# Kernel optimization log

Hardware: AMD Instinct MI355X
Metric: run time of the kernel (lower is better)

## Reference

```python
import jax, jax.numpy as jnp
import numpy as np

B, N, C = 32, 256, 4096
H = 16
HEAD_DIM = C // H  # 256 == N, required by the module's math
SCALE = HEAD_DIM ** -0.5


def setup_inputs() -> dict:
    key = jax.random.key(0)
    ks = jax.random.split(key, 7)
    std = C ** -0.5
    return {
        "x1": jax.random.normal(ks[0], (B, N, C), dtype=jnp.float32),
        "x2": jax.random.normal(ks[1], (B, N, C), dtype=jnp.float32),
        "Wq": jax.random.normal(ks[2], (C, C), dtype=jnp.float32) * std,
        "Wk": jax.random.normal(ks[3], (C, C), dtype=jnp.float32) * std,
        "Wv": jax.random.normal(ks[4], (C, C), dtype=jnp.float32) * std,
        "Wp": jax.random.normal(ks[5], (C, C), dtype=jnp.float32) * std,
        "bp": jnp.zeros((C,), dtype=jnp.float32),
    }


def reference(x1, x2, Wq, Wk, Wv, Wp, bp):
    b, n, c = x1.shape
    h, hd = H, HEAD_DIM
    # QKV projections (qkv_bias=False); q pre-scaled as in source
    q = (x1 @ Wq.T) * SCALE
    k = x2 @ Wk.T
    v = x2 @ Wv.T
    split = lambda t: t.reshape(b, n, h, hd).transpose(0, 2, 1, 3)  # b h n hd
    q, k, v = split(q), split(k), split(v)
    # channel-wise attention: q^T @ k over the token axis -> [b, h, hd, hd]
    attn = jax.nn.softmax(jnp.einsum("bhni,bhnj->bhij", q, k), axis=-1)
    # attn @ v: inner dim of attn (hd) contracts with token axis of v (n == hd)
    out = jnp.einsum("bhin,bhnc->bhic", attn, v)  # [b, h, hd, hd]
    out = out.transpose(0, 2, 1, 3).reshape(b, n, c)
    x = out @ Wp.T + bp
    return (x, attn)
```

## Files before the change

kernel.cpp:

```cpp
#include <hip/hip_runtime.h>

typedef __attribute__((ext_vector_type(4))) float f32x4;
typedef __attribute__((ext_vector_type(8))) short short8;
typedef __attribute__((ext_vector_type(4))) unsigned short ushort4v;

__device__ __forceinline__ unsigned short rne_bf16(float f) {
  unsigned int u = __builtin_bit_cast(unsigned int, f);
  u += 0x7FFFu + ((u >> 16) & 1u);
  return (unsigned short)(u >> 16);
}

__device__ __forceinline__ void async16(void* lds, const void* g) {
  __builtin_amdgcn_global_load_lds(
      (const __attribute__((address_space(1))) void*)g,
      (__attribute__((address_space(3))) void*)lds, 16, 0, 0);
}

__device__ __forceinline__ f32x4 mfma16(short8 a, short8 b, f32x4 c) {
  return __builtin_amdgcn_mfma_f32_16x16x32_bf16(a, b, c, 0, 0, 0);
}

__global__ __launch_bounds__(256) void cast_k(const float* __restrict__ in,
                                              unsigned short* __restrict__ out,
                                              int n4) {
  int stride = gridDim.x * 256;
  for (int i = blockIdx.x * 256 + threadIdx.x; i < n4; i += stride) {
    float4 v = ((const float4*)in)[i];
    ushort4v o = {rne_bf16(v.x), rne_bf16(v.y), rne_bf16(v.z), rne_bf16(v.w)};
    ((ushort4v*)out)[i] = o;
  }
}

__global__ __launch_bounds__(256) void cast_all(const float* __restrict__ x1,
                                                const float* __restrict__ x2,
                                                const float* __restrict__ Wq,
                                                const float* __restrict__ Wk,
                                                const float* __restrict__ Wv,
                                                const float* __restrict__ Wp,
                                                unsigned short* __restrict__ x1b,
                                                unsigned short* __restrict__ x2b,
                                                unsigned short* __restrict__ Wb4) {
  const int stride = gridDim.x * 256;
  for (int i = blockIdx.x * 256 + threadIdx.x; i < 33554432; i += stride) {
    const float* src;
    unsigned short* dst;
    int off;
    if (i < 8388608) {
      src = x1; dst = x1b; off = i;
    } else if (i < 16777216) {
      src = x2; dst = x2b; off = i - 8388608;
    } else {
      const int w = (i - 16777216) >> 22;
      off = (i - 16777216) & 4194303;
      src = (w == 0) ? Wq : (w == 1) ? Wk : (w == 2) ? Wv : Wp;
      dst = Wb4 + (size_t)w * 16777216;
    }
    float4 v = ((const float4*)src)[off];
    ushort4v o = {rne_bf16(v.x), rne_bf16(v.y), rne_bf16(v.z), rne_bf16(v.w)};
    ((ushort4v*)dst)[off] = o;
  }
}

template <int MODE>
__global__ __launch_bounds__(512, 2) void gemm256(const unsigned short* __restrict__ A1,
                                                  const unsigned short* __restrict__ A2,
                                                  const unsigned short* __restrict__ Bb,
                                                  size_t wstride,
                                                  float* __restrict__ outF,
                                                  unsigned short* __restrict__ outB0,
                                                  const float* __restrict__ bias,
                                                  int K, int lda, int ldb,
                                                  float scale0, float scale1, int gx) {
  __shared__ unsigned short lds[65536];
  const int tid = threadIdx.x;
  const int lane = tid & 63;
  const int wid = tid >> 6;
  const int wm = wid >> 2;
  const int wn = wid & 3;
  const int z = blockIdx.z;
  const unsigned short* A = z ? A2 : A1;
  const unsigned short* B = Bb + (size_t)z * wstride;
  unsigned short* outB = (MODE == 0) ? outB0 + (size_t)z * 33554432 : outB0;
  const float scale = z ? scale1 : scale0;
  int lin = blockIdx.x;
  lin = (lin & 7) * (gridDim.x >> 3) + (lin >> 3);
  const int bx = lin % gx;
  const int by = lin / gx;
  const int m0 = by * 256, n0 = bx * 256;
  const int NT = K >> 6;

  const int gsw8 = (((tid & 3) ^ ((tid >> 3) & 3))) * 8;
  const unsigned short* gA = A + (size_t)(m0 + (tid >> 2)) * lda + gsw8;
  const unsigned short* gB = B + (size_t)(n0 + (tid >> 2)) * ldb + gsw8;
  const size_t astep = (size_t)128 * lda;
  const size_t bstep = (size_t)128 * ldb;
  unsigned short* ld0 = &lds[tid * 8];

#define STG(Q) do { \
    const int kt_ = ((Q) >> 1) * 64 + ((Q) & 1) * 32; \
    const int off_ = (((Q) >> 1) & 1) * 32768 + ((Q) & 1) * 8192; \
    const unsigned short* sA_ = gA + kt_; \
    unsigned short* dA_ = ld0 + off_; \
    async16(dA_, sA_); async16(dA_ + 4096, sA_ + astep); \
    const unsigned short* sB_ = gB + kt_; \
    unsigned short* dB_ = ld0 + 16384 + off_; \
    async16(dB_, sB_); async16(dB_ + 4096, sB_ + bstep); } while (0)

  const int rl = lane & 15;
  const int ch = (lane >> 4) ^ ((rl >> 1) & 3);
  const int aidx = wm * 4096 + rl * 32 + ch * 8;
  const int bidx = 16384 + wn * 2048 + rl * 32 + ch * 8;

  short8 af[8], bf0[4], bf1[4];
#define READ_A(base) do { \
    _Pragma("unroll") \
    for (int r_ = 0; r_ < 8; ++r_) af[r_] = *(const short8*)&lds[(base) + aidx + r_ * 512]; \
  } while (0)
#define READ_B(base, dst) do { \
    _Pragma("unroll") \
    for (int s_ = 0; s_ < 4; ++s_) dst[s_] = *(const short8*)&lds[(base) + bidx + s_ * 512]; \
  } while (0)

  f32x4 acc[8][4];
#pragma unroll
  for (int r = 0; r < 8; ++r)
#pragma unroll
    for (int s = 0; s < 4; ++s) acc[r][s] = (f32x4){0.f, 0.f, 0.f, 0.f};

#define MFMA32(bfX) do { \
    __builtin_amdgcn_s_setprio(1); \
    _Pragma("unroll") \
    for (int r_ = 0; r_ < 8; ++r_) \
      _Pragma("unroll") \
      for (int s_ = 0; s_ < 4; ++s_) acc[r_][s_] = mfma16(af[r_], bfX[s_], acc[r_][s_]); \
    __builtin_amdgcn_s_setprio(0); \
  } while (0)

  STG(0); STG(1); STG(2);
  asm volatile("s_waitcnt vmcnt(4)" ::: "memory");
  __builtin_amdgcn_s_barrier();
  READ_B(0, bf0);

  for (int t = 0; t < NT; ++t) {
    const int bb = (t & 1) * 32768;
    READ_A(bb);
    READ_B(bb + 8192, bf1);
    if (t + 1 < NT) STG(2 * t + 3);
    __builtin_amdgcn_sched_barrier(0);
    MFMA32(bf0);
    if (t + 1 < NT) asm volatile("s_waitcnt vmcnt(4)" ::: "memory");
    else            asm volatile("s_waitcnt vmcnt(0)" ::: "memory");
    __builtin_amdgcn_s_barrier();
    READ_A(bb + 8192);
    if (t + 1 < NT) {
      READ_B(((t + 1) & 1) * 32768, bf0);
      if (t + 2 < NT) STG(2 * t + 4);
    }
    __builtin_amdgcn_sched_barrier(0);
    MFMA32(bf1);
    if (t + 1 < NT) {
      if (t + 2 < NT) asm volatile("s_waitcnt vmcnt(4)" ::: "memory");
      else            asm volatile("s_waitcnt vmcnt(0)" ::: "memory");
      __builtin_amdgcn_s_barrier();
    }
  }
#undef STG
#undef READ_A
#undef READ_B
#undef MFMA32

  const int fcol = lane & 15;
  const int frow = (lane >> 4) * 4;
#pragma unroll
  for (int r = 0; r < 8; ++r) {
#pragma unroll
    for (int s = 0; s < 4; ++s) {
      f32x4 v = acc[r][s];
      const int m = m0 + wm * 128 + r * 16 + frow;
      const int n = n0 + wn * 64 + s * 16 + fcol;
      if (MODE == 0) {
        ushort4v p;
#pragma unroll
        for (int j = 0; j < 4; ++j) p[j] = rne_bf16(v[j] * scale);
        size_t d = ((size_t)((m >> 8) * 16 + (n >> 8))) * 65536 +
                   (size_t)(n & 255) * 256 + (m & 255);
        *(ushort4v*)&outB[d] = p;
      } else {
        float bv = bias[n];
#pragma unroll
        for (int j = 0; j < 4; ++j) outF[(size_t)(m + j) * 4096 + n] = v[j] + bv;
      }
    }
  }
}

__global__ __launch_bounds__(256) void attn_fused(const unsigned short* __restrict__ Qt,
                                                  const unsigned short* __restrict__ Kt,
                                                  const unsigned short* __restrict__ Vt,
                                                  float* __restrict__ outA,
                                                  unsigned short* __restrict__ outXb) {
  __shared__ unsigned short sh[34560];
  const int tid = threadIdx.x;
  const int lane = tid & 63;
  const int wid = tid >> 6;
  const int z = blockIdx.y;
  const int m0 = blockIdx.x * 64;
  const int wm = wid >> 1;
  const int wn = wid & 1;
  const int fcol = lane & 15;
  const int kslot = (lane >> 4) * 8;
  const int frow = (lane >> 4) * 4;

  const unsigned short* Qh = Qt + (size_t)z * 65536;
  const unsigned short* Kh = Kt + (size_t)z * 65536;
  const unsigned short* Vh = Vt + (size_t)z * 65536;
  float* redM = (float*)&sh[33536];
  float* redS = redM + 128;

  f32x4 acc[2][8];
#pragma unroll
  for (int r = 0; r < 2; ++r)
#pragma unroll
    for (int s = 0; s < 8; ++s) acc[r][s] = (f32x4){0.f, 0.f, 0.f, 0.f};

  {
    const int arow = tid >> 2;
    const int acol = (tid & 3) * 8;
    const unsigned short* gQ = Qh + (size_t)(m0 + arow) * 256 + acol;
    const unsigned short* gK = Kh + (size_t)arow * 256 + acol;
    unsigned short* lA = &sh[tid * 8];
    unsigned short* lB = &sh[2048 + tid * 8];

    for (int kt = 0; kt < 256; kt += 32) {
      __syncthreads();
      async16(lA, gQ + kt);
      async16(lB, gK + kt);
      async16(lB + 2048, gK + (size_t)64 * 256 + kt);
      async16(lB + 4096, gK + (size_t)128 * 256 + kt);
      async16(lB + 6144, gK + (size_t)192 * 256 + kt);
      __syncthreads();

      short8 a[2], b[8];
#pragma unroll
      for (int r = 0; r < 2; ++r)
        a[r] = *(const short8*)&sh[(wm * 32 + r * 16 + fcol) * 32 + kslot];
#pragma unroll
      for (int s = 0; s < 8; ++s)
        b[s] = *(const short8*)&sh[2048 + (wn * 128 + s * 16 + fcol) * 32 + kslot];
#pragma unroll
      for (int r = 0; r < 2; ++r)
#pragma unroll
        for (int s = 0; s < 8; ++s)
          acc[r][s] = mfma16(a[r], b[s], acc[r][s]);
    }
  }
  __syncthreads();

#pragma unroll
  for (int r = 0; r < 2; ++r) {
#pragma unroll
    for (int j = 0; j < 4; ++j) {
      float m = acc[r][0][j];
#pragma unroll
      for (int s = 1; s < 8; ++s) m = fmaxf(m, acc[r][s][j]);
#pragma unroll
      for (int off = 1; off < 16; off <<= 1) m = fmaxf(m, __shfl_xor(m, off, 64));
      if (fcol == 0) redM[(wm * 32 + r * 16 + frow + j) * 2 + wn] = m;
    }
  }
  __syncthreads();
#pragma unroll
  for (int r = 0; r < 2; ++r) {
#pragma unroll
    for (int j = 0; j < 4; ++j) {
      const int rl = wm * 32 + r * 16 + frow + j;
      const float m = fmaxf(redM[rl * 2 + 0], redM[rl * 2 + 1]);
      float sum = 0.f;
#pragma unroll
      for (int s = 0; s < 8; ++s) {
        float e = __expf(acc[r][s][j] - m);
        acc[r][s][j] = e;
        sum += e;
      }
#pragma unroll
      for (int off = 1; off < 16; off <<= 1) sum += __shfl_xor(sum, off, 64);
      if (fcol == 0) redS[rl * 2 + wn] = sum;
    }
  }
  __syncthreads();
#pragma unroll
  for (int r = 0; r < 2; ++r) {
#pragma unroll
    for (int j = 0; j < 4; ++j) {
      const int rl = wm * 32 + r * 16 + frow + j;
      const float inv = 1.0f / (redS[rl * 2 + 0] + redS[rl * 2 + 1]);
      const size_t rowo = (size_t)z * 65536 + (size_t)(m0 + rl) * 256;
#pragma unroll
      for (int s = 0; s < 8; ++s) {
        const int col = wn * 128 + s * 16 + fcol;
        const float p = acc[r][s][j] * inv;
        outA[rowo + col] = p;
        sh[16384 + rl * 268 + col] = rne_bf16(p);
      }
    }
  }
  __syncthreads();

  const unsigned short* gV = Vh + (size_t)(tid >> 2) * 256 + (tid & 3) * 8;
#define STGV(kt, vb) do { \
    _Pragma("unroll") \
    for (int k_ = 0; k_ < 4; ++k_) \
      async16(&sh[(vb) + tid * 8 + k_ * 2048], \
              gV + (size_t)k_ * 64 * 256 + (kt) * 32); } while (0)

  STGV(0, 0); STGV(1, 8192);
  asm volatile("s_waitcnt vmcnt(4)" ::: "memory");
  __builtin_amdgcn_s_barrier();

  f32x4 acc2[2][8];
#pragma unroll
  for (int r = 0; r < 2; ++r)
#pragma unroll
    for (int s = 0; s < 8; ++s) acc2[r][s] = (f32x4){0.f, 0.f, 0.f, 0.f};

  for (int kt = 0; kt < 8; ++kt) {
    const int vb = (kt & 1) * 8192;
    short8 a2[2], b2[8];
#pragma unroll
    for (int r = 0; r < 2; ++r)
      a2[r] = *(const short8*)&sh[16384 + (wm * 32 + r * 16 + fcol) * 268 + kt * 32 + kslot];
#pragma unroll
    for (int s = 0; s < 8; ++s)
      b2[s] = *(const short8*)&sh[vb + (wn * 128 + s * 16 + fcol) * 32 + kslot];
#pragma unroll
    for (int r = 0; r < 2; ++r)
#pragma unroll
      for (int s = 0; s < 8; ++s)
        acc2[r][s] = mfma16(a2[r], b2[s], acc2[r][s]);
    __builtin_amdgcn_s_barrier();
    if (kt + 2 < 8) {
      STGV(kt + 2, vb);
      asm volatile("s_waitcnt vmcnt(4)" ::: "memory");
    } else {
      asm volatile("s_waitcnt vmcnt(0)" ::: "memory");
    }
    __builtin_amdgcn_s_barrier();
  }
#undef STGV

#pragma unroll
  for (int r = 0; r < 2; ++r) {
#pragma unroll
    for (int s = 0; s < 8; ++s) {
      f32x4 v = acc2[r][s];
      const int i0 = m0 + wm * 32 + r * 16 + frow;
      const int c = wn * 128 + s * 16 + fcol;
#pragma unroll
      for (int j = 0; j < 4; ++j) {
        size_t d = ((size_t)((z >> 4) * 256 + i0 + j)) * 4096 + (z & 15) * 256 + c;
        outXb[d] = rne_bf16(v[j]);
      }
    }
  }
}

extern "C" void kernel_launch(void* const* d_in, const int* in_sizes, int n_in,
                              void* d_out, int out_size, void* d_ws, size_t ws_size,
                              hipStream_t stream) {
  const float* x1 = (const float*)d_in[0];
  const float* x2 = (const float*)d_in[1];
  const float* Wq = (const float*)d_in[2];
  const float* Wk = (const float*)d_in[3];
  const float* Wv = (const float*)d_in[4];
  const float* Wp = (const float*)d_in[5];
  const float* bp = (const float*)d_in[6];

  float* outX = (float*)d_out;
  float* outA = outX + (size_t)33554432;

  unsigned short* Qt  = (unsigned short*)d_ws;
  unsigned short* Kt  = Qt + 33554432;
  unsigned short* Vt  = Kt + 33554432;
  unsigned short* x1b = Vt + 33554432;
  unsigned short* x2b = x1b + 33554432;

  const float SCALE = 0.0625f;
  const bool big = ws_size >= 469762048ULL;

  if (big) {
    unsigned short* Wb4 = x2b + 33554432;
    cast_all<<<2048, 256, 0, stream>>>(x1, x2, Wq, Wk, Wv, Wp, x1b, x2b, Wb4);
    gemm256<0><<<dim3(512, 1, 3), 512, 0, stream>>>(
        x1b, x2b, Wb4, (size_t)16777216, nullptr, Qt, nullptr,
        4096, 4096, 4096, SCALE, 1.0f, 16);
    attn_fused<<<dim3(4, 512), 256, 0, stream>>>(Qt, Kt, Vt, outA, x2b);
    gemm256<3><<<dim3(512, 1, 1), 512, 0, stream>>>(
        x2b, x2b, Wb4 + (size_t)50331648, 0, outX, nullptr, bp,
        4096, 4096, 4096, 1.0f, 1.0f, 16);
  } else {
    unsigned short* Wb = x2b + 33554432;
    cast_k<<<2048, 256, 0, stream>>>(x1, x1b, 8388608);
    cast_k<<<2048, 256, 0, stream>>>(x2, x2b, 8388608);
    cast_k<<<2048, 256, 0, stream>>>(Wq, Wb, 4194304);
    gemm256<0><<<dim3(512, 1, 1), 512, 0, stream>>>(
        x1b, x1b, Wb, 0, nullptr, Qt, nullptr, 4096, 4096, 4096, SCALE, SCALE, 16);
    cast_k<<<2048, 256, 0, stream>>>(Wk, Wb, 4194304);
    gemm256<0><<<dim3(512, 1, 1), 512, 0, stream>>>(
        x2b, x2b, Wb, 0, nullptr, Kt, nullptr, 4096, 4096, 4096, 1.0f, 1.0f, 16);
    cast_k<<<2048, 256, 0, stream>>>(Wv, Wb, 4194304);
    gemm256<0><<<dim3(512, 1, 1), 512, 0, stream>>>(
        x2b, x2b, Wb, 0, nullptr, Vt, nullptr, 4096, 4096, 4096, 1.0f, 1.0f, 16);
    attn_fused<<<dim3(4, 512), 256, 0, stream>>>(Qt, Kt, Vt, outA, x2b);
    cast_k<<<2048, 256, 0, stream>>>(Wp, Wb, 4194304);
    gemm256<3><<<dim3(512, 1, 1), 512, 0, stream>>>(
        x2b, x2b, Wb, 0, outX, nullptr, bp, 4096, 4096, 4096, 1.0f, 1.0f, 16);
  }
}
```

Measured before the change: 1.265 ms.

## Restructure GEMM main loop into quadrant-phased MFMA with split A/B staging

Reworks the bf16 GEMM inner loop so each 64-wide K step runs as four quadrant phases (4x2 MFMA tiles over both K halves). Each phase reads a smaller set of fragments from LDS and separates them with barriers. Global-to-LDS staging is split into separate A and B loads and issued between phases, and the prologue now prefetches four stages (vmcnt 8). The aim is to lower register pressure and interleave LDS reads with MFMA work. In exchange it adds more barriers per iteration and extra LDS-wait stalls.

```diff
diff --git a/kernel.cpp b/kernel.cpp
--- a/kernel.cpp
+++ b/kernel.cpp
@@ -96,14 +96,15 @@
   const size_t bstep = (size_t)128 * ldb;
   unsigned short* ld0 = &lds[tid * 8];
 
-#define STG(Q) do { \
-    const int kt_ = ((Q) >> 1) * 64 + ((Q) & 1) * 32; \
-    const int off_ = (((Q) >> 1) & 1) * 32768 + ((Q) & 1) * 8192; \
-    const unsigned short* sA_ = gA + kt_; \
-    unsigned short* dA_ = ld0 + off_; \
-    async16(dA_, sA_); async16(dA_ + 4096, sA_ + astep); \
-    const unsigned short* sB_ = gB + kt_; \
-    unsigned short* dB_ = ld0 + 16384 + off_; \
+#define ROFF(Q) ((((Q) >> 1) & 1) * 32768 + ((Q) & 1) * 8192)
+#define RKT(Q) (((Q) >> 1) * 64 + ((Q) & 1) * 32)
+#define STG_A(Q) do { \
+    const unsigned short* sA_ = gA + RKT(Q); \
+    unsigned short* dA_ = ld0 + ROFF(Q); \
+    async16(dA_, sA_); async16(dA_ + 4096, sA_ + astep); } while (0)
+#define STG_B(Q) do { \
+    const unsigned short* sB_ = gB + RKT(Q); \
+    unsigned short* dB_ = ld0 + 16384 + ROFF(Q); \
     async16(dB_, sB_); async16(dB_ + 4096, sB_ + bstep); } while (0)
 
   const int rl = lane & 15;
@@ -111,14 +112,16 @@
   const int aidx = wm * 4096 + rl * 32 + ch * 8;
   const int bidx = 16384 + wn * 2048 + rl * 32 + ch * 8;
 
-  short8 af[8], bf0[4], bf1[4];
-#define READ_A(base) do { \
+  short8 af0[4], af1[4], b00[2], b01[2], b10[2], b11[2];
+#define READ_A4(dst, base, q) do { \
     _Pragma("unroll") \
-    for (int r_ = 0; r_ < 8; ++r_) af[r_] = *(const short8*)&lds[(base) + aidx + r_ * 512]; \
+    for (int r_ = 0; r_ < 4; ++r_) \
+      dst[r_] = *(const short8*)&lds[(base) + aidx + ((q) * 4 + r_) * 512]; \
   } while (0)
-#define READ_B(base, dst) do { \
+#define READ_B2(dst, base, h) do { \
     _Pragma("unroll") \
-    for (int s_ = 0; s_ < 4; ++s_) dst[s_] = *(const short8*)&lds[(base) + bidx + s_ * 512]; \
+    for (int s_ = 0; s_ < 2; ++s_) \
+      dst[s_] = *(const short8*)&lds[(base) + bidx + ((h) * 2 + s_) * 512]; \
   } while (0)
 
   f32x4 acc[8][4];
@@ -127,47 +130,69 @@
 #pragma unroll
     for (int s = 0; s < 4; ++s) acc[r][s] = (f32x4){0.f, 0.f, 0.f, 0.f};
 
-#define MFMA32(bfX) do { \
+#define MFMAQ(bk0, bk1, ro, so) do { \
     __builtin_amdgcn_s_setprio(1); \
     _Pragma("unroll") \
-    for (int r_ = 0; r_ < 8; ++r_) \
+    for (int r_ = 0; r_ < 4; ++r_) \
       _Pragma("unroll") \
-      for (int s_ = 0; s_ < 4; ++s_) acc[r_][s_] = mfma16(af[r_], bfX[s_], acc[r_][s_]); \
+      for (int s_ = 0; s_ < 2; ++s_) { \
+        acc[(ro) + r_][(so) + s_] = mfma16(af0[r_], bk0[s_], acc[(ro) + r_][(so) + s_]); \
+        acc[(ro) + r_][(so) + s_] = mfma16(af1[r_], bk1[s_], acc[(ro) + r_][(so) + s_]); \
+      } \
     __builtin_amdgcn_s_setprio(0); \
   } while (0)
 
-  STG(0); STG(1); STG(2);
-  asm volatile("s_waitcnt vmcnt(4)" ::: "memory");
+#define PUBLISH() do { \
+    __builtin_amdgcn_s_barrier(); \
+    asm volatile("s_waitcnt lgkmcnt(0)" ::: "memory"); \
+    __builtin_amdgcn_sched_barrier(0); \
+  } while (0)
+
+  STG_A(0); STG_B(0); STG_A(1); STG_B(1);
+  STG_A(2); STG_B(2); STG_A(3); STG_B(3);
+  asm volatile("s_waitcnt vmcnt(8)" ::: "memory");
   __builtin_amdgcn_s_barrier();
-  READ_B(0, bf0);
 
   for (int t = 0; t < NT; ++t) {
-    const int bb = (t & 1) * 32768;
-    READ_A(bb);
-    READ_B(bb + 8192, bf1);
-    if (t + 1 < NT) STG(2 * t + 3);
-    __builtin_amdgcn_sched_barrier(0);
-    MFMA32(bf0);
-    if (t + 1 < NT) asm volatile("s_waitcnt vmcnt(4)" ::: "memory");
-    else            asm volatile("s_waitcnt vmcnt(0)" ::: "memory");
-    __builtin_amdgcn_s_barrier();
-    READ_A(bb + 8192);
-    if (t + 1 < NT) {
-      READ_B(((t + 1) & 1) * 32768, bf0);
-      if (t + 2 < NT) STG(2 * t + 4);
-    }
-    __builtin_amdgcn_sched_barrier(0);
-    MFMA32(bf1);
-    if (t + 1 < NT) {
-      if (t + 2 < NT) asm volatile("s_waitcnt vmcnt(4)" ::: "memory");
-      else            asm volatile("s_waitcnt vmcnt(0)" ::: "memory");
-      __builtin_amdgcn_s_barrier();
-    }
-  }
-#undef STG
-#undef READ_A
-#undef READ_B
-#undef MFMA32
+    const int rb0 = (t & 1) * 32768;
+    const int rb1 = rb0 + 8192;
+    const bool s2 = (t + 2) < NT;
+
+    READ_A4(af0, rb0, 0); READ_A4(af1, rb1, 0);
+    READ_B2(b00, rb0, 0); READ_B2(b01, rb1, 0);
+    PUBLISH();
+    MFMAQ(b00, b01, 0, 0);
+    __builtin_amdgcn_s_barrier();
+
+    READ_B2(b10, rb0, 1); READ_B2(b11, rb1, 1);
+    PUBLISH();
+    MFMAQ(b10, b11, 0, 2);
+    __builtin_amdgcn_s_barrier();
+
+    READ_A4(af0, rb0, 1); READ_A4(af1, rb1, 1);
+    if (s2) { STG_B(2 * t + 4); STG_B(2 * t + 5); }
+    PUBLISH();
+    MFMAQ(b00, b01, 4, 0);
+    __builtin_amdgcn_s_barrier();
+
+    if (s2) {
+      STG_A(2 * t + 4); STG_A(2 * t + 5);
+      asm volatile("s_waitcnt vmcnt(6)" ::: "memory");
+    } else if (t + 1 < NT) {
+      asm volatile("s_waitcnt vmcnt(0)" ::: "memory");
+    }
+    __builtin_amdgcn_s_barrier();
+    MFMAQ(b10, b11, 4, 2);
+    __builtin_amdgcn_s_barrier();
+  }
+#undef STG_A
+#undef STG_B
+#undef READ_A4
+#undef READ_B2
+#undef MFMAQ
+#undef PUBLISH
+#undef ROFF
+#undef RKT
 
   const int fcol = lane & 15;
   const int frow = (lane >> 4) * 4;
```

Result: slower. 1.302 ms (+3.0%).
